# Optimization experiments

Hardware: AMD Instinct MI355X
Metric: run time of the kernel (lower is better)

## Reference

```python
import jax, jax.numpy as jnp
import numpy as np

N_STREAMS = 4
DIM = 256
TMAX = 20
RMS_EPS = 1e-05
SK_EPS = 1e-08


def sinkhorn_knopp(logits):
    # logits: [B, T, n, n]; tmax fixed iterations of row/col normalization
    x = logits.astype(jnp.float32)
    x = x - jnp.max(x, axis=(-2, -1), keepdims=True)
    x = jnp.exp(x)
    for _ in range(TMAX):
        x = x / (jnp.sum(x, axis=-2, keepdims=True) + SK_EPS)
        x = x / (jnp.sum(x, axis=-1, keepdims=True) + SK_EPS)
    return x.astype(logits.dtype)


def setup_inputs() -> dict:
    key = jax.random.key(0)
    ks = jax.random.split(key, 5)
    B, T, n, C = 8, 4096, N_STREAMS, DIM
    nc = n * C
    x_streams = jax.random.normal(ks[0], (B, T, n, C), dtype=jnp.float32)
    scale = jnp.ones((nc,), dtype=jnp.float32)
    lim = 1.0 / np.sqrt(nc)
    w_pre = jax.random.uniform(ks[1], (n, nc), minval=-lim, maxval=lim, dtype=jnp.float32)
    w_post = jax.random.uniform(ks[2], (n, nc), minval=-lim, maxval=lim, dtype=jnp.float32)
    w_res = jax.random.uniform(ks[3], (n * n, nc), minval=-lim, maxval=lim, dtype=jnp.float32)
    return {
        "x_streams": x_streams,
        "scale": scale,
        "w_pre": w_pre,
        "w_post": w_post,
        "w_res": w_res,
        "alpha_pre": jnp.float32(0.01),
        "alpha_post": jnp.float32(0.01),
        "alpha_res": jnp.float32(0.01),
        "b_pre": jnp.zeros((n,), dtype=jnp.float32),
        "b_post": jnp.zeros((n,), dtype=jnp.float32),
        "b_res": jnp.zeros((n * n,), dtype=jnp.float32),
    }


def reference(x_streams, scale, w_pre, w_post, w_res,
              alpha_pre, alpha_post, alpha_res, b_pre, b_post, b_res):
    B, T, n, C = x_streams.shape
    x_flat = x_streams.reshape(B, T, n * C)
    # RMSNorm over flattened stream dim
    rms = jnp.mean(x_flat * x_flat, axis=-1, keepdims=True)
    x_norm = x_flat * jax.lax.rsqrt(rms + RMS_EPS) * scale
    # routing projections (Linear with no bias == x @ W.T)
    h_pre = jax.nn.sigmoid(alpha_pre * (x_norm @ w_pre.T) + b_pre)          # [B,T,n]
    h_post = 2.0 * jax.nn.sigmoid(alpha_post * (x_norm @ w_post.T) + b_post)  # [B,T,n]
    h_res = (alpha_res * (x_norm @ w_res.T) + b_res).reshape(B, T, n, n)
    h_res = sinkhorn_knopp(h_res)
    # mixing
    x_in = jnp.einsum('btn,btnc->btc', h_pre, x_streams)   # pre-mix (residual = Identity)
    y = x_in
    resmix = jnp.einsum('btij,btjc->btic', h_res, x_streams)
    addy = h_post[..., None] * y[..., None, :]
    return resmix + addy
```

## Files before the change

kernel.cpp:

```cpp
#include <hip/hip_runtime.h>
#include <math.h>

#define G 8

__device__ __forceinline__ float sigmoidf_(float s) {
    return 1.0f / (1.0f + __expf(-s));
}

__device__ __forceinline__ float fold_(float X, float Y, int m, int l) {
    const bool hi = (l & m) != 0;
    const float a = hi ? Y : X;
    const float b = hi ? X : Y;
    return a + __shfl_xor(b, m);
}

__device__ __forceinline__ void gll16(const float4* g, const float* lds) {
    __builtin_amdgcn_global_load_lds(
        (const __attribute__((address_space(1))) void*)g,
        (__attribute__((address_space(3))) void*)lds, 16, 0, 0);
}

__global__ __launch_bounds__(512)
__attribute__((amdgpu_waves_per_eu(4, 4)))
void fused_route_mix(const float* __restrict__ x,
                     const float* __restrict__ scale,
                     const float* __restrict__ w_pre,
                     const float* __restrict__ w_post,
                     const float* __restrict__ w_res,
                     const float* __restrict__ ap_p,
                     const float* __restrict__ apo_p,
                     const float* __restrict__ ar_p,
                     const float* __restrict__ b_pre,
                     const float* __restrict__ b_post,
                     const float* __restrict__ b_res,
                     float* __restrict__ out,
                     int rounds)
{
    __shared__ __align__(16) float xs[2][G * 1024];
    __shared__ __align__(16) float hraw[G * 24];
    __shared__ float sslds[G];
    __shared__ __align__(16) float Mlds[G * 16];

    const int t = threadIdx.x;
    const int w = t >> 6;
    const int l = t & 63;

    float wreg[3][16];
    #pragma unroll
    for (int rr = 0; rr < 3; ++rr) {
        const int k = 3 * w + rr;
        const float* wp = (k < 4) ? (w_pre + (size_t)k * 1024)
                        : (k < 8) ? (w_post + (size_t)(k - 4) * 1024)
                                  : (w_res + (size_t)(k - 8) * 1024);
        #pragma unroll
        for (int mp = 0; mp < 4; ++mp)
            #pragma unroll
            for (int j = 0; j < 4; ++j)
                wreg[rr][4 * mp + j] =
                    wp[4 * l + 256 * mp + j] * scale[4 * l + 256 * mp + j];
    }

    const int rstep = gridDim.x;
    int cur = 0;

    {
        const float4* __restrict__ xg =
            (const float4*)(x + (size_t)blockIdx.x * (G * 1024));
        #pragma unroll
        for (int i = 0; i < 4; ++i)
            gll16(xg + i * 512 + t, &xs[0][i * 2048 + (w << 8)]);
    }

    for (int r = blockIdx.x; r < rounds; r += rstep) {
        const size_t base = (size_t)r * (G * 1024);

        __syncthreads();

        const int rn = r + rstep;
        if (rn < rounds) {
            const float4* __restrict__ xg =
                (const float4*)(x + (size_t)rn * (G * 1024));
            #pragma unroll
            for (int i = 0; i < 4; ++i)
                gll16(xg + i * 512 + t, &xs[cur ^ 1][i * 2048 + (w << 8)]);
        }

        const float* __restrict__ xb = xs[cur];

        #pragma unroll 2
        for (int i = 0; i < G; ++i) {
            float p0 = 0.f, p1 = 0.f, p2 = 0.f, ss = 0.f;
            const float4* __restrict__ xi4 = (const float4*)(xb + i * 1024);
            #pragma unroll
            for (int mp = 0; mp < 4; ++mp) {
                const float4 xv = xi4[l + 64 * mp];
                const float xe[4] = {xv.x, xv.y, xv.z, xv.w};
                #pragma unroll
                for (int j = 0; j < 4; ++j) {
                    const float xj = xe[j];
                    p0 = fmaf(xj, wreg[0][4 * mp + j], p0);
                    p1 = fmaf(xj, wreg[1][4 * mp + j], p1);
                    p2 = fmaf(xj, wreg[2][4 * mp + j], p2);
                    ss = fmaf(xj, xj, ss);
                }
            }
            const float q0 = fold_(p0, p1, 32, l);
            const float q1 = fold_(p2, ss, 32, l);
            float s = fold_(q0, q1, 16, l);
            s += __shfl_xor(s, 8);
            s += __shfl_xor(s, 4);
            s += __shfl_xor(s, 2);
            s += __shfl_xor(s, 1);
            if ((l & 15) == 0) {
                const int vid = ((l >> 5) & 1) | (((l >> 4) & 1) << 1);
                if (vid < 3) hraw[i * 24 + 3 * w + vid] = s;
                else if (w == 0) sslds[i] = s;
            }
        }

        asm volatile("s_waitcnt lgkmcnt(0)\n\ts_barrier" ::: "memory");

        if (w == 0) {
            const int tk = l & (G - 1);
            const float inv = rsqrtf(sslds[tk] * (1.0f / 1024.0f) + 1e-5f);
            float hr[24];
            const float4* __restrict__ hp = (const float4*)(hraw + tk * 24);
            #pragma unroll
            for (int q = 0; q < 6; ++q) {
                const float4 hv = hp[q];
                hr[4 * q + 0] = hv.x; hr[4 * q + 1] = hv.y;
                hr[4 * q + 2] = hv.z; hr[4 * q + 3] = hv.w;
            }
            const float a_pre = ap_p[0], a_post = apo_p[0], a_res = ar_p[0];

            float hpre[4], hpost[4];
            #pragma unroll
            for (int j = 0; j < 4; ++j)
                hpre[j] = sigmoidf_(fmaf(a_pre * inv, hr[j], b_pre[j]));
            #pragma unroll
            for (int i = 0; i < 4; ++i)
                hpost[i] = 2.0f * sigmoidf_(fmaf(a_post * inv, hr[4 + i], b_post[i]));

            float K[4][4];
            float mx = -1e30f;
            #pragma unroll
            for (int i = 0; i < 4; ++i)
                #pragma unroll
                for (int j = 0; j < 4; ++j) {
                    const float vv = fmaf(a_res * inv, hr[8 + 4 * i + j], b_res[4 * i + j]);
                    K[i][j] = vv;
                    mx = fmaxf(mx, vv);
                }
            #pragma unroll
            for (int i = 0; i < 4; ++i)
                #pragma unroll
                for (int j = 0; j < 4; ++j)
                    K[i][j] = __expf(K[i][j] - mx);

            float u[4] = {1.f, 1.f, 1.f, 1.f};
            float v[4] = {1.f, 1.f, 1.f, 1.f};
            for (int it = 0; it < 20; ++it) {
                #pragma unroll
                for (int j = 0; j < 4; ++j) {
                    const float S = (fmaf(u[0], K[0][j], u[1] * K[1][j]))
                                  + (fmaf(u[2], K[2][j], u[3] * K[3][j]));
                    v[j] = v[j] * __builtin_amdgcn_rcpf(fmaf(v[j], S, 1e-8f));
                }
                #pragma unroll
                for (int i = 0; i < 4; ++i) {
                    const float T = (fmaf(K[i][0], v[0], K[i][1] * v[1]))
                                  + (fmaf(K[i][2], v[2], K[i][3] * v[3]));
                    u[i] = u[i] * __builtin_amdgcn_rcpf(fmaf(u[i], T, 1e-8f));
                }
            }

            if (l < G) {
                float4* Md = (float4*)(Mlds + (l << 4));
                #pragma unroll
                for (int i2 = 0; i2 < 4; ++i2) {
                    float4 row;
                    row.x = fmaf(u[i2] * K[i2][0], v[0], hpost[i2] * hpre[0]);
                    row.y = fmaf(u[i2] * K[i2][1], v[1], hpost[i2] * hpre[1]);
                    row.z = fmaf(u[i2] * K[i2][2], v[2], hpost[i2] * hpre[2]);
                    row.w = fmaf(u[i2] * K[i2][3], v[3], hpost[i2] * hpre[3]);
                    Md[i2] = row;
                }
            }
        }

        asm volatile("s_waitcnt lgkmcnt(0)\n\ts_barrier" ::: "memory");

        const int w4 = w & 3;
        const int half = t >> 8;
        #pragma unroll
        for (int ii = 0; ii < 4; ++ii) {
            const int i = 2 * ii + half;
            const float4 m4 = ((const float4*)Mlds)[(i << 2) + w4];
            const float4* __restrict__ xt = (const float4*)(xb + i * 1024);
            const float4 a0 = xt[0 * 64 + l];
            const float4 a1 = xt[1 * 64 + l];
            const float4 a2 = xt[2 * 64 + l];
            const float4 a3 = xt[3 * 64 + l];
            float4 o;
            o.x = m4.x * a0.x + m4.y * a1.x + m4.z * a2.x + m4.w * a3.x;
            o.y = m4.x * a0.y + m4.y * a1.y + m4.z * a2.y + m4.w * a3.y;
            o.z = m4.x * a0.z + m4.y * a1.z + m4.z * a2.z + m4.w * a3.z;
            o.w = m4.x * a0.w + m4.y * a1.w + m4.z * a2.w + m4.w * a3.w;
            ((float4*)(out + base))[(i << 8) + (w4 << 6) + l] = o;
        }

        cur ^= 1;
    }
}

extern "C" void kernel_launch(void* const* d_in, const int* in_sizes, int n_in,
                              void* d_out, int out_size, void* d_ws, size_t ws_size,
                              hipStream_t stream) {
    const float* x      = (const float*)d_in[0];
    const float* scale  = (const float*)d_in[1];
    const float* w_pre  = (const float*)d_in[2];
    const float* w_post = (const float*)d_in[3];
    const float* w_res  = (const float*)d_in[4];
    const float* a_pre  = (const float*)d_in[5];
    const float* a_post = (const float*)d_in[6];
    const float* a_res  = (const float*)d_in[7];
    const float* b_pre  = (const float*)d_in[8];
    const float* b_post = (const float*)d_in[9];
    const float* b_res  = (const float*)d_in[10];
    float* out = (float*)d_out;

    const int tokens = in_sizes[0] / 1024;
    const int rounds = tokens / G;
    const int grid = rounds < 512 ? rounds : 512;

    fused_route_mix<<<grid, 512, 0, stream>>>(
        x, scale, w_pre, w_post, w_res,
        a_pre, a_post, a_res, b_pre, b_post, b_res,
        out, rounds);
}
```

Measured before the change: 282.9 us.

## Halve block to 256 threads and 4 tokens, six projections per wave

Each block now handles 4 tokens per round with 256 threads instead of 8 tokens with 512 threads. Each wave holds six projection weight rows in registers instead of three, so four waves cover all 24 outputs. The shuffle reduction tree and the output indexing are reworked to match, and the grid is doubled to 1024 blocks. The aim is smaller blocks, lower LDS per block, more blocks in flight and cheaper barriers. The cost is higher register pressure from 96 weight registers per thread, which could cause spills or lower occupancy, and the waves_per_eu hint stays at 4.

```diff
diff --git a/kernel.cpp b/kernel.cpp
--- a/kernel.cpp
+++ b/kernel.cpp
@@ -1,7 +1,7 @@
 #include <hip/hip_runtime.h>
 #include <math.h>
 
-#define G 8
+#define G 4
 
 __device__ __forceinline__ float sigmoidf_(float s) {
     return 1.0f / (1.0f + __expf(-s));
@@ -20,7 +20,7 @@
         (__attribute__((address_space(3))) void*)lds, 16, 0, 0);
 }
 
-__global__ __launch_bounds__(512)
+__global__ __launch_bounds__(256)
 __attribute__((amdgpu_waves_per_eu(4, 4)))
 void fused_route_mix(const float* __restrict__ x,
                      const float* __restrict__ scale,
@@ -45,10 +45,10 @@
     const int w = t >> 6;
     const int l = t & 63;
 
-    float wreg[3][16];
+    float wreg[6][16];
     #pragma unroll
-    for (int rr = 0; rr < 3; ++rr) {
-        const int k = 3 * w + rr;
+    for (int rr = 0; rr < 6; ++rr) {
+        const int k = 6 * w + rr;
         const float* wp = (k < 4) ? (w_pre + (size_t)k * 1024)
                         : (k < 8) ? (w_post + (size_t)(k - 4) * 1024)
                                   : (w_res + (size_t)(k - 8) * 1024);
@@ -60,6 +60,8 @@
                     wp[4 * l + 256 * mp + j] * scale[4 * l + 256 * mp + j];
     }
 
+    const float a_pre = ap_p[0], a_post = apo_p[0], a_res = ar_p[0];
+
     const int rstep = gridDim.x;
     int cur = 0;
 
@@ -67,8 +69,8 @@
         const float4* __restrict__ xg =
             (const float4*)(x + (size_t)blockIdx.x * (G * 1024));
         #pragma unroll
-        for (int i = 0; i < 4; ++i)
-            gll16(xg + i * 512 + t, &xs[0][i * 2048 + (w << 8)]);
+        for (int i = 0; i < G; ++i)
+            gll16(xg + i * 256 + (w << 6) + l, &xs[0][i * 1024 + (w << 8)]);
     }
 
     for (int r = blockIdx.x; r < rounds; r += rstep) {
@@ -81,15 +83,16 @@
             const float4* __restrict__ xg =
                 (const float4*)(x + (size_t)rn * (G * 1024));
             #pragma unroll
-            for (int i = 0; i < 4; ++i)
-                gll16(xg + i * 512 + t, &xs[cur ^ 1][i * 2048 + (w << 8)]);
+            for (int i = 0; i < G; ++i)
+                gll16(xg + i * 256 + (w << 6) + l, &xs[cur ^ 1][i * 1024 + (w << 8)]);
         }
 
         const float* __restrict__ xb = xs[cur];
 
         #pragma unroll 2
         for (int i = 0; i < G; ++i) {
-            float p0 = 0.f, p1 = 0.f, p2 = 0.f, ss = 0.f;
+            float p0 = 0.f, p1 = 0.f, p2 = 0.f, p3 = 0.f, p4 = 0.f, p5 = 0.f;
+            float ss = 0.f;
             const float4* __restrict__ xi4 = (const float4*)(xb + i * 1024);
             #pragma unroll
             for (int mp = 0; mp < 4; ++mp) {
@@ -101,20 +104,26 @@
                     p0 = fmaf(xj, wreg[0][4 * mp + j], p0);
                     p1 = fmaf(xj, wreg[1][4 * mp + j], p1);
                     p2 = fmaf(xj, wreg[2][4 * mp + j], p2);
+                    p3 = fmaf(xj, wreg[3][4 * mp + j], p3);
+                    p4 = fmaf(xj, wreg[4][4 * mp + j], p4);
+                    p5 = fmaf(xj, wreg[5][4 * mp + j], p5);
                     ss = fmaf(xj, xj, ss);
                 }
             }
             const float q0 = fold_(p0, p1, 32, l);
-            const float q1 = fold_(p2, ss, 32, l);
-            float s = fold_(q0, q1, 16, l);
-            s += __shfl_xor(s, 8);
+            const float q1 = fold_(p2, p3, 32, l);
+            const float q2 = fold_(p4, p5, 32, l);
+            const float q3 = ss + __shfl_xor(ss, 32);
+            const float r0v = fold_(q0, q1, 16, l);
+            const float r1v = fold_(q2, q3, 16, l);
+            float s = fold_(r0v, r1v, 8, l);
             s += __shfl_xor(s, 4);
             s += __shfl_xor(s, 2);
             s += __shfl_xor(s, 1);
-            if ((l & 15) == 0) {
-                const int vid = ((l >> 5) & 1) | (((l >> 4) & 1) << 1);
-                if (vid < 3) hraw[i * 24 + 3 * w + vid] = s;
-                else if (w == 0) sslds[i] = s;
+            if ((l & 7) == 0) {
+                const int vid = ((l >> 3) & 1) * 4 + ((l >> 4) & 1) * 2 + ((l >> 5) & 1);
+                if (vid < 6) hraw[i * 24 + 6 * w + vid] = s;
+                else if (w == 0 && vid == 6) sslds[i] = s;
             }
         }
 
@@ -131,7 +140,6 @@
                 hr[4 * q + 0] = hv.x; hr[4 * q + 1] = hv.y;
                 hr[4 * q + 2] = hv.z; hr[4 * q + 3] = hv.w;
             }
-            const float a_pre = ap_p[0], a_post = apo_p[0], a_res = ar_p[0];
 
             float hpre[4], hpost[4];
             #pragma unroll
@@ -190,12 +198,9 @@
 
         asm volatile("s_waitcnt lgkmcnt(0)\n\ts_barrier" ::: "memory");
 
-        const int w4 = w & 3;
-        const int half = t >> 8;
         #pragma unroll
-        for (int ii = 0; ii < 4; ++ii) {
-            const int i = 2 * ii + half;
-            const float4 m4 = ((const float4*)Mlds)[(i << 2) + w4];
+        for (int i = 0; i < G; ++i) {
+            const float4 m4 = ((const float4*)Mlds)[(i << 2) + w];
             const float4* __restrict__ xt = (const float4*)(xb + i * 1024);
             const float4 a0 = xt[0 * 64 + l];
             const float4 a1 = xt[1 * 64 + l];
@@ -206,7 +211,7 @@
             o.y = m4.x * a0.y + m4.y * a1.y + m4.z * a2.y + m4.w * a3.y;
             o.z = m4.x * a0.z + m4.y * a1.z + m4.z * a2.z + m4.w * a3.z;
             o.w = m4.x * a0.w + m4.y * a1.w + m4.z * a2.w + m4.w * a3.w;
-            ((float4*)(out + base))[(i << 8) + (w4 << 6) + l] = o;
+            ((float4*)(out + base))[(i << 8) + (w << 6) + l] = o;
         }
 
         cur ^= 1;
@@ -231,9 +236,9 @@
 
     const int tokens = in_sizes[0] / 1024;
     const int rounds = tokens / G;
-    const int grid = rounds < 512 ? rounds : 512;
-
-    fused_route_mix<<<grid, 512, 0, stream>>>(
+    const int grid = rounds < 1024 ? rounds : 1024;
+
+    fused_route_mix<<<grid, 256, 0, stream>>>(
         x, scale, w_pre, w_post, w_res,
         a_pre, a_post, a_res, b_pre, b_post, b_res,
         out, rounds);
```

Result: slower. 535.9 us (+89.4%).

## Load x directly from global in projection pass and stage single LDS buffer

Applied to the files above, without the earlier changes.

Removes the double-buffered global_load_lds prefetch and instead has every wave read x rows straight from global memory during the projection/RMS pass. Each wave copies its assigned two rows into a single LDS buffer for later reuse by the mixing pass. The group size doubles from 8 to 16 tokens per round, and the alpha scalars are hoisted out of the loop. This trades explicit cross-round prefetch overlap for larger per-block work and simpler loads, relying on occupancy and the cache to hide latency. Each x row is now fetched redundantly by all eight waves, which adds L2 traffic.

```diff
diff --git a/kernel.cpp b/kernel.cpp
--- a/kernel.cpp
+++ b/kernel.cpp
@@ -1,7 +1,7 @@
 #include <hip/hip_runtime.h>
 #include <math.h>
 
-#define G 8
+#define G 16
 
 __device__ __forceinline__ float sigmoidf_(float s) {
     return 1.0f / (1.0f + __expf(-s));
@@ -12,12 +12,6 @@
     const float a = hi ? Y : X;
     const float b = hi ? X : Y;
     return a + __shfl_xor(b, m);
-}
-
-__device__ __forceinline__ void gll16(const float4* g, const float* lds) {
-    __builtin_amdgcn_global_load_lds(
-        (const __attribute__((address_space(1))) void*)g,
-        (__attribute__((address_space(3))) void*)lds, 16, 0, 0);
 }
 
 __global__ __launch_bounds__(512)
@@ -36,7 +30,7 @@
                      float* __restrict__ out,
                      int rounds)
 {
-    __shared__ __align__(16) float xs[2][G * 1024];
+    __shared__ __align__(16) float xs[G * 1024];
     __shared__ __align__(16) float hraw[G * 24];
     __shared__ float sslds[G];
     __shared__ __align__(16) float Mlds[G * 16];
@@ -60,40 +54,24 @@
                     wp[4 * l + 256 * mp + j] * scale[4 * l + 256 * mp + j];
     }
 
-    const int rstep = gridDim.x;
-    int cur = 0;
-
-    {
-        const float4* __restrict__ xg =
-            (const float4*)(x + (size_t)blockIdx.x * (G * 1024));
-        #pragma unroll
-        for (int i = 0; i < 4; ++i)
-            gll16(xg + i * 512 + t, &xs[0][i * 2048 + (w << 8)]);
-    }
-
-    for (int r = blockIdx.x; r < rounds; r += rstep) {
+    const float a_pre = ap_p[0], a_post = apo_p[0], a_res = ar_p[0];
+    float4* const xs4 = (float4*)xs;
+
+    for (int r = blockIdx.x; r < rounds; r += gridDim.x) {
         const size_t base = (size_t)r * (G * 1024);
-
-        __syncthreads();
-
-        const int rn = r + rstep;
-        if (rn < rounds) {
-            const float4* __restrict__ xg =
-                (const float4*)(x + (size_t)rn * (G * 1024));
-            #pragma unroll
-            for (int i = 0; i < 4; ++i)
-                gll16(xg + i * 512 + t, &xs[cur ^ 1][i * 2048 + (w << 8)]);
-        }
-
-        const float* __restrict__ xb = xs[cur];
+        const float4* __restrict__ xg = (const float4*)(x + base);
+
+        asm volatile("s_waitcnt lgkmcnt(0)\n\ts_barrier" ::: "memory");
 
         #pragma unroll 2
         for (int i = 0; i < G; ++i) {
             float p0 = 0.f, p1 = 0.f, p2 = 0.f, ss = 0.f;
-            const float4* __restrict__ xi4 = (const float4*)(xb + i * 1024);
+            const bool stage = ((i >> 1) == w);
             #pragma unroll
             for (int mp = 0; mp < 4; ++mp) {
-                const float4 xv = xi4[l + 64 * mp];
+                const float4 xv = xg[(i << 8) + (mp << 6) + l];
+                if (stage)
+                    xs4[(i << 8) + (mp << 6) + l] = xv;
                 const float xe[4] = {xv.x, xv.y, xv.z, xv.w};
                 #pragma unroll
                 for (int j = 0; j < 4; ++j) {
@@ -131,7 +109,6 @@
                 hr[4 * q + 0] = hv.x; hr[4 * q + 1] = hv.y;
                 hr[4 * q + 2] = hv.z; hr[4 * q + 3] = hv.w;
             }
-            const float a_pre = ap_p[0], a_post = apo_p[0], a_res = ar_p[0];
 
             float hpre[4], hpost[4];
             #pragma unroll
@@ -190,13 +167,13 @@
 
         asm volatile("s_waitcnt lgkmcnt(0)\n\ts_barrier" ::: "memory");
 
-        const int w4 = w & 3;
-        const int half = t >> 8;
-        #pragma unroll
-        for (int ii = 0; ii < 4; ++ii) {
-            const int i = 2 * ii + half;
-            const float4 m4 = ((const float4*)Mlds)[(i << 2) + w4];
-            const float4* __restrict__ xt = (const float4*)(xb + i * 1024);
+        const int s4 = w & 3;
+        const int ihalf = w >> 2;
+        #pragma unroll 2
+        for (int ii = 0; ii < 8; ++ii) {
+            const int i = (ii << 1) + ihalf;
+            const float4 m4 = ((const float4*)Mlds)[(i << 2) + s4];
+            const float4* __restrict__ xt = xs4 + (i << 8);
             const float4 a0 = xt[0 * 64 + l];
             const float4 a1 = xt[1 * 64 + l];
             const float4 a2 = xt[2 * 64 + l];
@@ -206,10 +183,8 @@
             o.y = m4.x * a0.y + m4.y * a1.y + m4.z * a2.y + m4.w * a3.y;
             o.z = m4.x * a0.z + m4.y * a1.z + m4.z * a2.z + m4.w * a3.z;
             o.w = m4.x * a0.w + m4.y * a1.w + m4.z * a2.w + m4.w * a3.w;
-            ((float4*)(out + base))[(i << 8) + (w4 << 6) + l] = o;
+            ((float4*)(out + base))[(i << 8) + (s4 << 6) + l] = o;
         }
-
-        cur ^= 1;
     }
 }
 
```

After: 290.1 us. 1.03x slower.
